# Kernel optimization log

Measured on AMD Instinct MI355X. Metric: run time of the kernel, lower is better.

## Reference

```python
import jax, jax.numpy as jnp
import numpy as np

NUM_HEADS = 4
HEAD_DIM = 32
QUERY_DIM = 256
KEY_DIM = 128
INNER = NUM_HEADS * HEAD_DIM  # 128


def setup_inputs() -> dict:
    key = jax.random.key(0)
    ks = jax.random.split(key, 8)
    B, T, D, H, W = 2, 4, QUERY_DIM, 40, 40
    C, Hm, Wm = KEY_DIM, 40, 40
    query = jax.random.normal(ks[0], (B, T, D, H, W), dtype=jnp.float32)
    k_in = jax.random.normal(ks[1], (B, T, C, Hm, Wm), dtype=jnp.float32)
    v_in = jax.random.normal(ks[2], (B, T, C, Hm, Wm), dtype=jnp.float32)
    # Linear weights stored as (in, out); torch nn.Linear init ~ U(-1/sqrt(in), 1/sqrt(in))
    def lin(k, fan_in, fan_out):
        bound = 1.0 / np.sqrt(fan_in)
        return jax.random.uniform(k, (fan_in, fan_out), minval=-bound, maxval=bound, dtype=jnp.float32)
    Wq = lin(ks[3], QUERY_DIM, INNER)
    Wk = lin(ks[4], KEY_DIM, INNER)
    Wv = lin(ks[5], KEY_DIM, INNER)
    Wo = lin(ks[6], INNER, QUERY_DIM)
    bo = jax.random.uniform(ks[7], (QUERY_DIM,), minval=-1.0 / np.sqrt(INNER), maxval=1.0 / np.sqrt(INNER), dtype=jnp.float32)
    return {"query": query, "key": k_in, "value": v_in,
            "Wq": Wq, "Wk": Wk, "Wv": Wv, "Wo": Wo, "bo": bo}


def reference(query, key, value, Wq, Wk, Wv, Wo, bo):
    B, T, D, H, W = query.shape
    _, _, C, Hm, Wm = key.shape
    scale = HEAD_DIM ** (-0.5)
    # b t d h w -> b t (h w) d
    q = query.reshape(B, T, D, H * W).transpose(0, 1, 3, 2)
    k = key.reshape(B, T, C, Hm * Wm).transpose(0, 1, 3, 2)
    v = value.reshape(B, T, C, Hm * Wm).transpose(0, 1, 3, 2)
    # projections then split heads: b t n (h d) -> b t h n d
    def heads(x):
        Bn, Tn, N, _ = x.shape
        return x.reshape(Bn, Tn, N, NUM_HEADS, HEAD_DIM).transpose(0, 1, 3, 2, 4)
    Q = heads(q @ Wq)
    K = heads(k @ Wk)
    V = heads(v @ Wv)
    scores = jnp.einsum('bthqd,bthkd->bthqk', Q, K) * scale
    probs = jax.nn.softmax(scores, axis=-1)
    out = jnp.einsum('bthqk,bthkd->bthqd', probs, V)
    # b t h n d -> b t n (h d)
    out = out.transpose(0, 1, 3, 2, 4).reshape(B, T, H * W, INNER)
    fused = out @ Wo + bo
    # b t (h w) d -> b t d h w
    return fused.transpose(0, 1, 3, 2).reshape(B, T, D, H, W)
```

## Files before the change

### kernel.cpp

```cpp
#include <hip/hip_runtime.h>

#define NTOK 1600
#define BT_TOTAL 8
#define INNER 128
#define HD 32
#define NH 4
#define QDIM 256

typedef short short8 __attribute__((ext_vector_type(8)));
typedef short short4v __attribute__((ext_vector_type(4)));
typedef float f32x4 __attribute__((ext_vector_type(4)));
typedef float f32x16 __attribute__((ext_vector_type(16)));

__device__ inline short f2b(float x) {
  union { float f; unsigned u; } v; v.f = x;
  unsigned r = (v.u + 0x7FFF + ((v.u >> 16) & 1)) >> 16;
  return (short)r;
}
__device__ inline unsigned bpack2(float a, float b) {
  union { float f; unsigned u; } ua, ub;
  ua.f = a; ub.f = b;
  return __builtin_amdgcn_perm(ub.u + 0x8000u, ua.u + 0x8000u, 0x07060302u);
}
__device__ inline short8 ldsfrag(const short* p) {
  short4v a = *(const short4v*)p;
  short4v b = *(const short4v*)(p + 4);
  short8 r;
  r[0] = a[0]; r[1] = a[1]; r[2] = a[2]; r[3] = a[3];
  r[4] = b[0]; r[5] = b[1]; r[6] = b[2]; r[7] = b[3];
  return r;
}
__device__ inline short8 mk8(unsigned a, unsigned b, unsigned c, unsigned d) {
  union { unsigned u[4]; short8 v; } t;
  t.u[0] = a; t.u[1] = b; t.u[2] = c; t.u[3] = d;
  return t.v;
}

__global__ __launch_bounds__(256) void proj_fused(
    const float* __restrict__ query, const float* __restrict__ Wq,
    const float* __restrict__ key, const float* __restrict__ Wk,
    const float* __restrict__ value, const float* __restrict__ Wv,
    short* __restrict__ Qbf, short* __restrict__ Kbf,
    short* __restrict__ Vbf) {
  const int n0 = blockIdx.x * 64;
  const int which = blockIdx.y;
  const int bt = blockIdx.z;
  const int t = threadIdx.x;
  const int lane = t & 63, w = t >> 6;
  const int quad = lane >> 4, n16 = lane & 15;

  const float* X; const float* Wt; short* Y; int nchunk; float scl;
  if (which == 0) {
    X = query; Wt = Wq; Y = Qbf; nchunk = 8; scl = 0.17677669529663687f;
  } else if (which == 1) {
    X = key; Wt = Wk; Y = Kbf; nchunk = 4; scl = 1.0f;
  } else {
    X = value; Wt = Wv; Y = Vbf; nchunk = 4; scl = 1.0f;
  }
  const float* Xb = X + (size_t)bt * (nchunk * 32) * NTOK;

  __shared__ short Xs[64 * 36];
  __shared__ short Ws[128 * 36];

  f32x4 acc[8];
#pragma unroll
  for (int i = 0; i < 8; ++i) acc[i] = (f32x4){0.f, 0.f, 0.f, 0.f};

  const int iw = t & 127, g = t >> 7;

  float xf0[4], xf1[4], wf0[8], wf1[8];
  auto loadX = [&](int cd) {
#pragma unroll
    for (int dp = 0; dp < 4; ++dp) {
      int dl = w * 8 + dp * 2;
      xf0[dp] = Xb[(size_t)(cd + dl) * NTOK + n0 + lane];
      xf1[dp] = Xb[(size_t)(cd + dl + 1) * NTOK + n0 + lane];
    }
  };
  auto loadW = [&](int cd) {
#pragma unroll
    for (int dp = 0; dp < 8; ++dp) {
      int dl = g * 16 + dp * 2;
      wf0[dp] = Wt[(size_t)(cd + dl) * INNER + iw];
      wf1[dp] = Wt[(size_t)(cd + dl + 1) * INNER + iw];
    }
  };
  loadX(0); loadW(0);

  for (int c = 0; c < nchunk; ++c) {
#pragma unroll
    for (int dp = 0; dp < 4; ++dp)
      *(unsigned*)&Xs[lane * 36 + w * 8 + dp * 2] = bpack2(xf0[dp], xf1[dp]);
#pragma unroll
    for (int dp = 0; dp < 8; ++dp)
      *(unsigned*)&Ws[iw * 36 + g * 16 + dp * 2] = bpack2(wf0[dp], wf1[dp]);
    __syncthreads();
    if (c + 1 < nchunk) { loadX((c + 1) * 32); loadW((c + 1) * 32); }
    if (which != 2) {
      short8 a[4], b[2];
#pragma unroll
      for (int tg = 0; tg < 4; ++tg)
        a[tg] = ldsfrag(&Xs[(tg * 16 + n16) * 36 + quad * 8]);
#pragma unroll
      for (int cg = 0; cg < 2; ++cg)
        b[cg] = ldsfrag(&Ws[(w * 32 + cg * 16 + n16) * 36 + quad * 8]);
#pragma unroll
      for (int tg = 0; tg < 4; ++tg)
#pragma unroll
        for (int cg = 0; cg < 2; ++cg)
          acc[tg * 2 + cg] = __builtin_amdgcn_mfma_f32_16x16x32_bf16(
              a[tg], b[cg], acc[tg * 2 + cg], 0, 0, 0);
    } else {
      short8 a[2], b[4];
#pragma unroll
      for (int ig = 0; ig < 2; ++ig)
        a[ig] = ldsfrag(&Ws[(w * 32 + ig * 16 + n16) * 36 + quad * 8]);
#pragma unroll
      for (int tg = 0; tg < 4; ++tg)
        b[tg] = ldsfrag(&Xs[(tg * 16 + n16) * 36 + quad * 8]);
#pragma unroll
      for (int ig = 0; ig < 2; ++ig)
#pragma unroll
        for (int tg = 0; tg < 4; ++tg)
          acc[ig * 4 + tg] = __builtin_amdgcn_mfma_f32_16x16x32_bf16(
              a[ig], b[tg], acc[ig * 4 + tg], 0, 0, 0);
    }
    __syncthreads();
  }

  if (which != 2) {
    short* Yb = Y + ((size_t)bt * NH + w) * NTOK * HD;
#pragma unroll
    for (int tg = 0; tg < 4; ++tg)
#pragma unroll
      for (int cg = 0; cg < 2; ++cg) {
        f32x4 a = acc[tg * 2 + cg];
#pragma unroll
        for (int r = 0; r < 4; ++r) {
          int tok = n0 + tg * 16 + quad * 4 + r;
          Yb[(size_t)tok * HD + cg * 16 + n16] = f2b(a[r] * scl);
        }
      }
  } else {
#pragma unroll
    for (int ig = 0; ig < 2; ++ig)
#pragma unroll
      for (int tg = 0; tg < 4; ++tg) {
        f32x4 a = acc[ig * 4 + tg];
#pragma unroll
        for (int r = 0; r < 4; ++r) {
          int irow = w * 32 + ig * 16 + quad * 4 + r;
          Y[((size_t)bt * INNER + irow) * NTOK + n0 + tg * 16 + n16] =
              f2b(a[r]);
        }
      }
  }
}

__global__ __launch_bounds__(256, 5) void attn_mfma(
    const short* __restrict__ Qb, const short* __restrict__ Kb,
    const short* __restrict__ Vb, short* __restrict__ Obf) {
  const int id = blockIdx.x;
  const int qt = id >> 5;
  const int pair = id & 31;
  const int bt = pair >> 2, h = pair & 3;
  const int wave = threadIdx.x >> 6, lane = threadIdx.x & 63;
  const int lh = lane >> 5, q32 = lane & 31;
  const int q0 = qt * 32;
  const size_t btok = ((size_t)bt * NH + h) * NTOK;
  const size_t bd = ((size_t)bt * NH + h) * HD;
  const bool hi = (lane >= 32);

  __shared__ float Cb[2][17][64];

  const short* Qp = &Qb[(btok + q0 + q32) * HD + lh * 8];
  const short8 bq0 = *(const short8*)(Qp);
  const short8 bq1 = *(const short8*)(Qp + 16);

  const int kstart = wave * 416 - (wave == 3 ? 32 : 0);
  const int nch = 13 - (wave >> 1);
  const short* Kp = &Kb[(btok + kstart + q32) * HD + lh * 8];
  const short* Vp = &Vb[(bd + q32) * NTOK + kstart + lh * 8];

  f32x16 o = {0.f, 0.f, 0.f, 0.f, 0.f, 0.f, 0.f, 0.f,
              0.f, 0.f, 0.f, 0.f, 0.f, 0.f, 0.f, 0.f};
  float lsum = 0.f;

  short8 ak0 = *(const short8*)(Kp);
  short8 ak1 = *(const short8*)(Kp + 16);

  for (int i = 0; i < nch; ++i) {
    const int kc = i * 32;
    const int kn = (i + 1 < nch) ? kc + 32 : 0;
    short8 nk0 = *(const short8*)(Kp + (size_t)kn * HD);
    short8 nk1 = *(const short8*)(Kp + (size_t)kn * HD + 16);
    short8 av0 = *(const short8*)(Vp + kc);
    short8 av1 = *(const short8*)(Vp + kc + 16);

    f32x16 s = __builtin_amdgcn_mfma_f32_32x32x16_bf16(
        ak0, bq0,
        (f32x16){0.f, 0.f, 0.f, 0.f, 0.f, 0.f, 0.f, 0.f,
                 0.f, 0.f, 0.f, 0.f, 0.f, 0.f, 0.f, 0.f},
        0, 0, 0);
    s = __builtin_amdgcn_mfma_f32_32x32x16_bf16(ak1, bq1, s, 0, 0, 0);

    unsigned Pd[8];
#pragma unroll
    for (int g = 0; g < 4; ++g) {
      float e0 = __expf(s[4 * g + 0]);
      float e1 = __expf(s[4 * g + 1]);
      float e2 = __expf(s[4 * g + 2]);
      float e3 = __expf(s[4 * g + 3]);
      lsum += (e0 + e1) + (e2 + e3);
      Pd[2 * g + 0] = bpack2(e0, e1);
      Pd[2 * g + 1] = bpack2(e2, e3);
    }
    unsigned Xd[8];
#pragma unroll
    for (int j = 0; j < 8; ++j)
      Xd[j] = (unsigned)__shfl_xor((int)Pd[j], 32);
    short8 pb0 = mk8(hi ? Xd[2] : Pd[0], hi ? Xd[3] : Pd[1],
                     hi ? Pd[2] : Xd[0], hi ? Pd[3] : Xd[1]);
    short8 pb1 = mk8(hi ? Xd[6] : Pd[4], hi ? Xd[7] : Pd[5],
                     hi ? Pd[6] : Xd[4], hi ? Pd[7] : Xd[5]);

    o = __builtin_amdgcn_mfma_f32_32x32x16_bf16(av0, pb0, o, 0, 0, 0);
    o = __builtin_amdgcn_mfma_f32_32x32x16_bf16(av1, pb1, o, 0, 0, 0);
    ak0 = nk0; ak1 = nk1;
  }

  lsum += __shfl_xor(lsum, 32);

  auto dump = [&](int sidx) {
#pragma unroll
    for (int r = 0; r < 16; ++r) Cb[sidx][r][lane] = o[r];
    Cb[sidx][16][lane] = lsum;
  };
  auto accum = [&](int sidx) {
#pragma unroll
    for (int r = 0; r < 16; ++r) o[r] += Cb[sidx][r][lane];
    lsum += Cb[sidx][16][lane];
  };
  if (wave == 1) dump(0);
  if (wave == 3) dump(1);
  __syncthreads();
  if (wave == 0) accum(0);
  if (wave == 2) accum(1);
  __syncthreads();
  if (wave == 2) dump(0);
  __syncthreads();
  if (wave == 0) {
    accum(0);
    const float inv = 1.f / lsum;
    short* Op = &Obf[((size_t)bt * NTOK + q0 + q32) * INNER + h * HD + lh * 4];
#pragma unroll
    for (int g = 0; g < 4; ++g) {
      unsigned d0 = bpack2(o[4 * g + 0] * inv, o[4 * g + 1] * inv);
      unsigned d1 = bpack2(o[4 * g + 2] * inv, o[4 * g + 3] * inv);
      *(uint2*)&Op[8 * g] = make_uint2(d0, d1);
    }
  }
}

__global__ __launch_bounds__(256) void oproj_mfma(
    const short* __restrict__ Obf, const float* __restrict__ Wo,
    const float* __restrict__ bo, float* __restrict__ out) {
  const int tok0 = blockIdx.x * 64, d0 = blockIdx.y * 64;
  const int bt = blockIdx.z;
  const int t = threadIdx.x, lane = t & 63, w = t >> 6;
  const int quad = lane >> 4, n16 = lane & 15;
  __shared__ short Wos[64 * 36];
  f32x4 acc[4];
#pragma unroll
  for (int i = 0; i < 4; ++i) acc[i] = (f32x4){0.f, 0.f, 0.f, 0.f};
  const int tok = tok0 + w * 16 + n16;

  float wf0[4], wf1[4];
  short8 bfr;
  auto loadWo = [&](int c) {
#pragma unroll
    for (int dp = 0; dp < 4; ++dp) {
      int il = w * 8 + dp * 2;
      wf0[dp] = Wo[(size_t)(c * 32 + il) * QDIM + d0 + lane];
      wf1[dp] = Wo[(size_t)(c * 32 + il + 1) * QDIM + d0 + lane];
    }
  };
  auto loadB = [&](int c) {
    bfr = *(const short8*)&Obf[((size_t)bt * NTOK + tok) * INNER + c * 32 +
                               quad * 8];
  };
  loadWo(0); loadB(0);

  for (int c = 0; c < 4; ++c) {
#pragma unroll
    for (int dp = 0; dp < 4; ++dp)
      *(unsigned*)&Wos[lane * 36 + w * 8 + dp * 2] = bpack2(wf0[dp], wf1[dp]);
    __syncthreads();
    short8 b0 = bfr;
    if (c < 3) { loadWo(c + 1); loadB(c + 1); }
#pragma unroll
    for (int ag = 0; ag < 4; ++ag) {
      short8 a = ldsfrag(&Wos[(ag * 16 + n16) * 36 + quad * 8]);
      acc[ag] = __builtin_amdgcn_mfma_f32_16x16x32_bf16(a, b0, acc[ag], 0, 0, 0);
    }
    __syncthreads();
  }

#pragma unroll
  for (int ag = 0; ag < 4; ++ag) {
    f32x4 a = acc[ag];
#pragma unroll
    for (int r = 0; r < 4; ++r) {
      int dout = d0 + ag * 16 + quad * 4 + r;
      out[((size_t)bt * QDIM + dout) * NTOK + tok] = a[r] + bo[dout];
    }
  }
}

extern "C" void kernel_launch(void* const* d_in, const int* in_sizes, int n_in,
                              void* d_out, int out_size, void* d_ws,
                              size_t ws_size, hipStream_t stream) {
  const float* query = (const float*)d_in[0];
  const float* key = (const float*)d_in[1];
  const float* value = (const float*)d_in[2];
  const float* Wq = (const float*)d_in[3];
  const float* Wk = (const float*)d_in[4];
  const float* Wv = (const float*)d_in[5];
  const float* Wo = (const float*)d_in[6];
  const float* bo = (const float*)d_in[7];
  float* out = (float*)d_out;

  const size_t arr = (size_t)BT_TOTAL * INNER * NTOK;
  short* Qbf = (short*)d_ws;
  short* Kbf = Qbf + arr;
  short* Vbf = Kbf + arr;
  short* Obf = Vbf + arr;

  proj_fused<<<dim3(25, 3, BT_TOTAL), 256, 0, stream>>>(
      query, Wq, key, Wk, value, Wv, Qbf, Kbf, Vbf);
  attn_mfma<<<dim3(1600), 256, 0, stream>>>(Qbf, Kbf, Vbf, Obf);
  oproj_mfma<<<dim3(25, 4, BT_TOTAL), 256, 0, stream>>>(Obf, Wo, bo, out);
}
```

Measured before the change: 132.4 us.

## Use native bf16 pack, exp2 with folded log2e, permlane swap, and V prefetch

Replaces the software bf16 rounding/perm with the hardware v_cvt_pk_bf16_f32 instruction, folds log2(e) into the Q scale so softmax uses raw exp2, and swaps the 8 shfl_xor plus select sequence for permlane32_swap. It also prefetches V one iteration ahead like K, accumulates the row sum with packed float2 adds, and raises wave priority around the MFMAs. These cut VALU and cross-lane work in the attention inner loop, at the cost of more live registers from the extra V prefetch under the occupancy-5 launch bound.

```diff
diff --git a/kernel.cpp b/kernel.cpp
--- a/kernel.cpp
+++ b/kernel.cpp
@@ -9,18 +9,24 @@
 
 typedef short short8 __attribute__((ext_vector_type(8)));
 typedef short short4v __attribute__((ext_vector_type(4)));
+typedef float f32x2 __attribute__((ext_vector_type(2)));
 typedef float f32x4 __attribute__((ext_vector_type(4)));
 typedef float f32x16 __attribute__((ext_vector_type(16)));
+typedef unsigned uint2v __attribute__((ext_vector_type(2)));
 
 __device__ inline short f2b(float x) {
   union { float f; unsigned u; } v; v.f = x;
   unsigned r = (v.u + 0x7FFF + ((v.u >> 16) & 1)) >> 16;
   return (short)r;
 }
-__device__ inline unsigned bpack2(float a, float b) {
-  union { float f; unsigned u; } ua, ub;
-  ua.f = a; ub.f = b;
-  return __builtin_amdgcn_perm(ub.u + 0x8000u, ua.u + 0x8000u, 0x07060302u);
+__device__ inline unsigned cvtpk(float a, float b) {
+  unsigned r;
+  asm("v_cvt_pk_bf16_f32 %0, %1, %2" : "=v"(r) : "v"(a), "v"(b));
+  return r;
+}
+__device__ inline void pswap(unsigned &a, unsigned &b) {
+  uint2v r = __builtin_amdgcn_permlane32_swap(a, b, false, false);
+  a = r[0]; b = r[1];
 }
 __device__ inline short8 ldsfrag(const short* p) {
   short4v a = *(const short4v*)p;
@@ -51,7 +57,8 @@
 
   const float* X; const float* Wt; short* Y; int nchunk; float scl;
   if (which == 0) {
-    X = query; Wt = Wq; Y = Qbf; nchunk = 8; scl = 0.17677669529663687f;
+    X = query; Wt = Wq; Y = Qbf; nchunk = 8;
+    scl = 0.17677669529663687f * 1.4426950408889634f;
   } else if (which == 1) {
     X = key; Wt = Wk; Y = Kbf; nchunk = 4; scl = 1.0f;
   } else {
@@ -90,10 +97,10 @@
   for (int c = 0; c < nchunk; ++c) {
 #pragma unroll
     for (int dp = 0; dp < 4; ++dp)
-      *(unsigned*)&Xs[lane * 36 + w * 8 + dp * 2] = bpack2(xf0[dp], xf1[dp]);
+      *(unsigned*)&Xs[lane * 36 + w * 8 + dp * 2] = cvtpk(xf0[dp], xf1[dp]);
 #pragma unroll
     for (int dp = 0; dp < 8; ++dp)
-      *(unsigned*)&Ws[iw * 36 + g * 16 + dp * 2] = bpack2(wf0[dp], wf1[dp]);
+      *(unsigned*)&Ws[iw * 36 + g * 16 + dp * 2] = cvtpk(wf0[dp], wf1[dp]);
     __syncthreads();
     if (c + 1 < nchunk) { loadX((c + 1) * 32); loadW((c + 1) * 32); }
     if (which != 2) {
@@ -169,7 +176,6 @@
   const int q0 = qt * 32;
   const size_t btok = ((size_t)bt * NH + h) * NTOK;
   const size_t bd = ((size_t)bt * NH + h) * HD;
-  const bool hi = (lane >= 32);
 
   __shared__ float Cb[2][17][64];
 
@@ -184,51 +190,57 @@
 
   f32x16 o = {0.f, 0.f, 0.f, 0.f, 0.f, 0.f, 0.f, 0.f,
               0.f, 0.f, 0.f, 0.f, 0.f, 0.f, 0.f, 0.f};
-  float lsum = 0.f;
+  f32x2 ls2 = {0.f, 0.f};
 
   short8 ak0 = *(const short8*)(Kp);
   short8 ak1 = *(const short8*)(Kp + 16);
+  short8 av0 = *(const short8*)(Vp);
+  short8 av1 = *(const short8*)(Vp + 16);
 
   for (int i = 0; i < nch; ++i) {
-    const int kc = i * 32;
-    const int kn = (i + 1 < nch) ? kc + 32 : 0;
+    const int kn = (i + 1 < nch) ? (i + 1) * 32 : 0;
     short8 nk0 = *(const short8*)(Kp + (size_t)kn * HD);
     short8 nk1 = *(const short8*)(Kp + (size_t)kn * HD + 16);
-    short8 av0 = *(const short8*)(Vp + kc);
-    short8 av1 = *(const short8*)(Vp + kc + 16);
-
+    short8 nv0 = *(const short8*)(Vp + kn);
+    short8 nv1 = *(const short8*)(Vp + kn + 16);
+
+    __builtin_amdgcn_s_setprio(1);
     f32x16 s = __builtin_amdgcn_mfma_f32_32x32x16_bf16(
         ak0, bq0,
         (f32x16){0.f, 0.f, 0.f, 0.f, 0.f, 0.f, 0.f, 0.f,
                  0.f, 0.f, 0.f, 0.f, 0.f, 0.f, 0.f, 0.f},
         0, 0, 0);
     s = __builtin_amdgcn_mfma_f32_32x32x16_bf16(ak1, bq1, s, 0, 0, 0);
+    __builtin_amdgcn_s_setprio(0);
 
     unsigned Pd[8];
 #pragma unroll
     for (int g = 0; g < 4; ++g) {
-      float e0 = __expf(s[4 * g + 0]);
-      float e1 = __expf(s[4 * g + 1]);
-      float e2 = __expf(s[4 * g + 2]);
-      float e3 = __expf(s[4 * g + 3]);
-      lsum += (e0 + e1) + (e2 + e3);
-      Pd[2 * g + 0] = bpack2(e0, e1);
-      Pd[2 * g + 1] = bpack2(e2, e3);
-    }
-    unsigned Xd[8];
-#pragma unroll
-    for (int j = 0; j < 8; ++j)
-      Xd[j] = (unsigned)__shfl_xor((int)Pd[j], 32);
-    short8 pb0 = mk8(hi ? Xd[2] : Pd[0], hi ? Xd[3] : Pd[1],
-                     hi ? Pd[2] : Xd[0], hi ? Pd[3] : Xd[1]);
-    short8 pb1 = mk8(hi ? Xd[6] : Pd[4], hi ? Xd[7] : Pd[5],
-                     hi ? Pd[6] : Xd[4], hi ? Pd[7] : Xd[5]);
-
+      float e0 = __builtin_amdgcn_exp2f(s[4 * g + 0]);
+      float e1 = __builtin_amdgcn_exp2f(s[4 * g + 1]);
+      float e2 = __builtin_amdgcn_exp2f(s[4 * g + 2]);
+      float e3 = __builtin_amdgcn_exp2f(s[4 * g + 3]);
+      ls2 += (f32x2){e0, e1};
+      ls2 += (f32x2){e2, e3};
+      Pd[2 * g + 0] = cvtpk(e0, e1);
+      Pd[2 * g + 1] = cvtpk(e2, e3);
+    }
+    pswap(Pd[0], Pd[2]);
+    pswap(Pd[1], Pd[3]);
+    pswap(Pd[4], Pd[6]);
+    pswap(Pd[5], Pd[7]);
+    short8 pb0 = mk8(Pd[0], Pd[1], Pd[2], Pd[3]);
+    short8 pb1 = mk8(Pd[4], Pd[5], Pd[6], Pd[7]);
+
+    __builtin_amdgcn_s_setprio(1);
     o = __builtin_amdgcn_mfma_f32_32x32x16_bf16(av0, pb0, o, 0, 0, 0);
     o = __builtin_amdgcn_mfma_f32_32x32x16_bf16(av1, pb1, o, 0, 0, 0);
-    ak0 = nk0; ak1 = nk1;
-  }
-
+    __builtin_amdgcn_s_setprio(0);
+
+    ak0 = nk0; ak1 = nk1; av0 = nv0; av1 = nv1;
+  }
+
+  float lsum = ls2[0] + ls2[1];
   lsum += __shfl_xor(lsum, 32);
 
   auto dump = [&](int sidx) {
@@ -255,8 +267,8 @@
     short* Op = &Obf[((size_t)bt * NTOK + q0 + q32) * INNER + h * HD + lh * 4];
 #pragma unroll
     for (int g = 0; g < 4; ++g) {
-      unsigned d0 = bpack2(o[4 * g + 0] * inv, o[4 * g + 1] * inv);
-      unsigned d1 = bpack2(o[4 * g + 2] * inv, o[4 * g + 3] * inv);
+      unsigned d0 = cvtpk(o[4 * g + 0] * inv, o[4 * g + 1] * inv);
+      unsigned d1 = cvtpk(o[4 * g + 2] * inv, o[4 * g + 3] * inv);
       *(uint2*)&Op[8 * g] = make_uint2(d0, d1);
     }
   }
@@ -294,7 +306,7 @@
   for (int c = 0; c < 4; ++c) {
 #pragma unroll
     for (int dp = 0; dp < 4; ++dp)
-      *(unsigned*)&Wos[lane * 36 + w * 8 + dp * 2] = bpack2(wf0[dp], wf1[dp]);
+      *(unsigned*)&Wos[lane * 36 + w * 8 + dp * 2] = cvtpk(wf0[dp], wf1[dp]);
     __syncthreads();
     short8 b0 = bfr;
     if (c < 3) { loadWo(c + 1); loadB(c + 1); }
```

Result: no change. 133.3 us (+0.7%).
